# Optimization experiments

Hardware: AMD Instinct MI355X
Metric: run time of the kernel (lower is better)

The kernel has to match this reference:

```python
import jax, jax.numpy as jnp
import numpy as np

B, DIM, L, H, W = 4, 128, 256, 8, 8
N = L * H * W
D_INNER, D_STATE, D_CONV, DT_RANK = 128, 8, 4, 8


def _ln(x, w, b, eps=1e-5):
    m = x.mean(-1, keepdims=True)
    v = ((x - m) ** 2).mean(-1, keepdims=True)
    return (x - m) * jax.lax.rsqrt(v + eps) * w + b


def _mamba_fusion(x, z_in, p, i):
    # x, z_in: (B, N, DIM). x drives the SSM; z_in provides the cross-modal gate.
    u = x @ p['Wx'][i]                                    # (B, N, D_INNER)
    z = z_in @ p['Wz'][i]                                 # (B, N, D_INNER)
    # causal depthwise conv1d along tokens, kernel D_CONV (torch pad=k-1 then truncate)
    up = jnp.pad(u, ((0, 0), (D_CONV - 1, 0), (0, 0)))
    w = p['conv_w'][i]                                    # (D_INNER, D_CONV)
    uc = sum(up[:, k:k + u.shape[1], :] * w[:, k] for k in range(D_CONV)) + p['conv_b'][i]
    uc = jax.nn.silu(uc)
    x_dbl = uc @ p['Wxproj'][i]                           # (B, N, DT_RANK + 2*D_STATE)
    dt_r, Bm, Cm = jnp.split(x_dbl, [DT_RANK, DT_RANK + D_STATE], axis=-1)
    dt = jax.nn.softplus(dt_r @ p['Wdt'][i] + p['bdt'][i])  # (B, N, D_INNER)
    A = -jnp.exp(p['A_log'][i])                           # (D_INNER, D_STATE)
    dA = jnp.exp(dt[..., None] * A)                       # (B, N, D_INNER, D_STATE)
    dBu = dt[..., None] * Bm[:, :, None, :] * uc[..., None]

    def step(h, inp):
        dA_t, dBu_t, C_t = inp
        h = dA_t * h + dBu_t                              # (B, D_INNER, D_STATE)
        return h, jnp.einsum('bds,bs->bd', h, C_t)

    h0 = jnp.zeros((u.shape[0], D_INNER, D_STATE), u.dtype)
    _, ys = jax.lax.scan(step, h0, (dA.swapaxes(0, 1), dBu.swapaxes(0, 1), Cm.swapaxes(0, 1)))
    y = ys.swapaxes(0, 1) + p['Dp'][i] * uc
    y = y * jax.nn.silu(z)
    return y @ p['Wout_m'][i] + p['bout_m'][i]


def _cross_block(in0, in1, p, i):
    skip = in0
    a = _ln(in0, p['ln0_w'][i], p['ln0_b'][i])
    b = _ln(in1, p['ln1_w'][i], p['ln1_b'][i])
    return skip + _mamba_fusion(a, b, p, i)


def setup_inputs() -> dict:
    key = jax.random.key(0)
    ks = jax.random.split(key, 16)
    s_in = 1.0 / np.sqrt(DIM)
    s_di = 1.0 / np.sqrt(D_INNER)
    inp = {
        'front': jax.random.normal(ks[0], (B, DIM, L, H, W), jnp.float32),
        'back': jax.random.normal(ks[1], (B, DIM, L, H, W), jnp.float32),
        'ln0_w': jnp.ones((2, DIM), jnp.float32),
        'ln0_b': jnp.zeros((2, DIM), jnp.float32),
        'ln1_w': jnp.ones((2, DIM), jnp.float32),
        'ln1_b': jnp.zeros((2, DIM), jnp.float32),
        'Wx': jax.random.normal(ks[2], (2, DIM, D_INNER), jnp.float32) * s_in,
        'Wz': jax.random.normal(ks[3], (2, DIM, D_INNER), jnp.float32) * s_in,
        'conv_w': jax.random.normal(ks[4], (2, D_INNER, D_CONV), jnp.float32) * 0.5,
        'conv_b': jnp.zeros((2, D_INNER), jnp.float32),
        'Wxproj': jax.random.normal(ks[5], (2, D_INNER, DT_RANK + 2 * D_STATE), jnp.float32) * s_di,
        'Wdt': jax.random.normal(ks[6], (2, DT_RANK, D_INNER), jnp.float32) * (1.0 / np.sqrt(DT_RANK)),
        'bdt': jnp.full((2, D_INNER), -4.6, jnp.float32),  # softplus^-1(~0.01)
        'A_log': jnp.broadcast_to(jnp.log(jnp.arange(1, D_STATE + 1, dtype=jnp.float32)), (2, D_INNER, D_STATE)).copy(),
        'Dp': jnp.ones((2, D_INNER), jnp.float32),
        'Wout_m': jax.random.normal(ks[7], (2, D_INNER, DIM), jnp.float32) * s_di,
        'bout_m': jnp.zeros((2, DIM), jnp.float32),
        'Wout': jax.random.normal(ks[8], (DIM, DIM), jnp.float32) * s_in,
        'bout': jnp.zeros((DIM,), jnp.float32),
    }
    return inp


def reference(front, back, ln0_w, ln0_b, ln1_w, ln1_b, Wx, Wz, conv_w, conv_b,
              Wxproj, Wdt, bdt, A_log, Dp, Wout_m, bout_m, Wout, bout):
    p = dict(ln0_w=ln0_w, ln0_b=ln0_b, ln1_w=ln1_w, ln1_b=ln1_b, Wx=Wx, Wz=Wz,
             conv_w=conv_w, conv_b=conv_b, Wxproj=Wxproj, Wdt=Wdt, bdt=bdt,
             A_log=A_log, Dp=Dp, Wout_m=Wout_m, bout_m=bout_m)
    ff = front.reshape(B, DIM, N).swapaxes(1, 2)          # (B, N, DIM)
    bf = back.reshape(B, DIM, N).swapaxes(1, 2)
    f_fus = _cross_block(ff, bf, p, 0)
    b_fus = _cross_block(bf, ff, p, 1)
    fusion = ((f_fus + b_fus) * 0.5) @ Wout + bout
    return fusion.swapaxes(1, 2).reshape(B, DIM, L, H, W)
```

## Files before the change

### kernel.cpp

```cpp
#include <hip/hip_runtime.h>

#define DEV static __device__ __forceinline__

typedef short s16x8 __attribute__((ext_vector_type(8)));
typedef float f32x4 __attribute__((ext_vector_type(4)));
typedef unsigned short u16;

DEV float b2f(u16 u){ return __uint_as_float(((unsigned int)u) << 16); }
DEV u16 f2b(float f){
  unsigned int x = __float_as_uint(f);
  x += 0x7fffu + ((x >> 16) & 1u);
  return (u16)(x >> 16);
}
DEV float silu_f(float x){ return x * __builtin_amdgcn_rcpf(1.f + __expf(-x)); }
DEV float softplus_f(float x){ return (x > 15.f) ? x : __logf(1.f + __expf(x)); }
DEV bool detf32(const void* lnw){ return *(const unsigned int*)lnw == 0x3F800000u; }
DEV float ldin(const void* p, long long i, bool f){
  return f ? ((const float*)p)[i] : b2f(((const u16*)p)[i]);
}

static constexpr int BATCH = 4;
static constexpr int NSEQ  = 16384;
static constexpr int RTOT  = BATCH * NSEQ;
static constexpr int GCH   = 256;
static constexpr int DIRSZ = BATCH*GCH*128*8;

__global__ __launch_bounds__(256) void k_setup(
                        const void* ln0w, const void* ln0b, const void* ln1w, const void* ln1b,
                        const void* Wx, const void* Wz, const void* Wxp, const void* Wdt,
                        const void* bdt, const void* Alog, const void* convw, const void* convb,
                        const void* Dpr, const void* Woutm, const void* boutm,
                        const void* Wout, const void* bout,
                        u16* Wuz, u16* WdtBC, u16* Wcat, u16* WoutT,
                        float* buz, float* bdtf, float* bcat, float* boutf,
                        float* Aexp, float* convwF, float* convbF, float* DpF)
{
  bool f = detf32(ln0w);
  int tid = blockIdx.x * 256 + threadIdx.x;
  int gs  = gridDim.x * 256;
  for (int idx = tid; idx < 2*256*128; idx += gs){
    int d = idx >> 15; int n = (idx >> 7) & 255; int k = idx & 127;
    float wv;
    if (n < 128) wv = ldin(ln0w, d*128+k, f) * ldin(Wx, (long long)(d*128+k)*128 + n, f);
    else         wv = ldin(ln1w, (1-d)*128+k, f) * ldin(Wz, (long long)((1-d)*128+k)*128 + (n-128), f);
    Wuz[idx] = f2b(wv);
  }
  for (int idx = tid; idx < 2*256; idx += gs){
    int d = idx >> 8; int n = idx & 255;
    float s = 0.f;
    if (n < 128){
      for (int k = 0; k < 128; ++k)
        s += ldin(ln0b, d*128+k, f) * ldin(Wx, (long long)(d*128+k)*128 + n, f);
    } else {
      for (int k = 0; k < 128; ++k)
        s += ldin(ln1b, (1-d)*128+k, f) * ldin(Wz, (long long)((1-d)*128+k)*128 + (n-128), f);
    }
    buz[idx] = s;
  }
  for (int idx = tid; idx < 2*128; idx += gs)
    bdtf[idx] = ldin(bdt, idx, f);
  for (int idx = tid; idx < 2*144*128; idx += gs){
    int i = idx / (144*128); int rem = idx % (144*128); int n = rem >> 7; int k = rem & 127;
    if (n < 128){
      float s = 0.f;
      for (int j = 0; j < 8; ++j)
        s += ldin(Wxp, (long long)(i*128+k)*24 + j, f) * ldin(Wdt, (long long)(i*8+j)*128 + n, f);
      WdtBC[idx] = f2b(s);
    } else {
      WdtBC[idx] = f2b(ldin(Wxp, (long long)(i*128+k)*24 + (n - 120), f));
    }
  }
  for (int idx = tid; idx < 128*256; idx += gs){
    int n = idx >> 8; int k = idx & 255;
    Wcat[idx] = f2b(ldin(Woutm, (long long)k*128 + n, f));
  }
  for (int idx = tid; idx < 128*128; idx += gs){
    int n = idx >> 7, k = idx & 127;
    WoutT[idx] = f2b(ldin(Wout, (long long)k*128 + n, f));
  }
  for (int idx = tid; idx < 128; idx += gs){
    bcat[idx]  = ldin(boutm, idx, f) + ldin(boutm, 128 + idx, f);
    boutf[idx] = ldin(bout, idx, f);
  }
  for (int idx = tid; idx < 2*128*8; idx += gs)
    Aexp[idx] = -expf(ldin(Alog, idx, f));
  for (int idx = tid; idx < 2*128*4; idx += gs)
    convwF[idx] = ldin(convw, idx, f);
  for (int idx = tid; idx < 2*128; idx += gs){
    convbF[idx] = ldin(convb, idx, f);
    DpF[idx]   = ldin(Dpr, idx, f);
  }
}

__global__ __launch_bounds__(256) void k_ln(const void* front, const void* back, const void* ln0w,
                                            u16* xf, u16* xb, u16* sfbh)
{
  bool fF = detf32(ln0w);
  __shared__ u16 Af[64][130];
  __shared__ u16 Ab[64][130];
  __shared__ float Mf[64], Rf[64], Mb[64], Rb[64];
  int tid = threadIdx.x;
  long long r0 = (long long)blockIdx.x * 64;
  int b  = (int)(r0 >> 14);
  int n0 = (int)(r0 & 16383);
  if (fF){
    const float* fp = (const float*)front;
    const float* bp = (const float*)back;
    for (int it = 0; it < 8; ++it){
      int d = it*16 + (tid >> 4);
      int t = (tid & 15) * 4;
      long long gi = ((long long)(b*128 + d))*NSEQ + n0 + t;
      float4 vf = *(const float4*)&fp[gi];
      float4 vb = *(const float4*)&bp[gi];
      Af[t+0][d] = f2b(vf.x); Af[t+1][d] = f2b(vf.y);
      Af[t+2][d] = f2b(vf.z); Af[t+3][d] = f2b(vf.w);
      Ab[t+0][d] = f2b(vb.x); Ab[t+1][d] = f2b(vb.y);
      Ab[t+2][d] = f2b(vb.z); Ab[t+3][d] = f2b(vb.w);
    }
  } else {
    const u16* fp = (const u16*)front;
    const u16* bp = (const u16*)back;
    for (int it = 0; it < 4; ++it){
      int d = it*32 + (tid >> 3);
      int t = (tid & 7) * 8;
      long long gi = ((long long)(b*128 + d))*NSEQ + n0 + t;
      uint4 vf = *(const uint4*)&fp[gi];
      uint4 vb = *(const uint4*)&bp[gi];
      Af[t+0][d] = (u16)vf.x; Af[t+1][d] = (u16)(vf.x>>16);
      Af[t+2][d] = (u16)vf.y; Af[t+3][d] = (u16)(vf.y>>16);
      Af[t+4][d] = (u16)vf.z; Af[t+5][d] = (u16)(vf.z>>16);
      Af[t+6][d] = (u16)vf.w; Af[t+7][d] = (u16)(vf.w>>16);
      Ab[t+0][d] = (u16)vb.x; Ab[t+1][d] = (u16)(vb.x>>16);
      Ab[t+2][d] = (u16)vb.y; Ab[t+3][d] = (u16)(vb.y>>16);
      Ab[t+4][d] = (u16)vb.z; Ab[t+5][d] = (u16)(vb.z>>16);
      Ab[t+6][d] = (u16)vb.w; Ab[t+7][d] = (u16)(vb.w>>16);
    }
  }
  __syncthreads();
  {
    int t = tid >> 2, sub = tid & 3;
    float s = 0.f, ss = 0.f, s2 = 0.f, ss2 = 0.f;
    for (int k = 0; k < 32; ++k){
      float v = b2f(Af[t][sub*32 + k]); s  += v; ss  += v*v;
      float w = b2f(Ab[t][sub*32 + k]); s2 += w; ss2 += w*w;
    }
    for (int m = 1; m < 4; m <<= 1){
      s  += __shfl_xor(s,  m, 64); ss  += __shfl_xor(ss,  m, 64);
      s2 += __shfl_xor(s2, m, 64); ss2 += __shfl_xor(ss2, m, 64);
    }
    if (sub == 0){
      float mf = s  * (1.f/128.f); float vf = ss  * (1.f/128.f) - mf*mf;
      Mf[t] = mf; Rf[t] = rsqrtf(vf + 1e-5f);
      float mb = s2 * (1.f/128.f); float vb = ss2 * (1.f/128.f) - mb*mb;
      Mb[t] = mb; Rb[t] = rsqrtf(vb + 1e-5f);
    }
  }
  __syncthreads();
  for (int it = 0; it < 8; ++it){
    int t = it*8 + (tid >> 5);
    int c = (tid & 31) * 4;
    float mf = Mf[t], rf = Rf[t], mb = Mb[t], rb = Rb[t];
    float f0 = b2f(Af[t][c+0]), f1 = b2f(Af[t][c+1]), f2 = b2f(Af[t][c+2]), f3 = b2f(Af[t][c+3]);
    float g0 = b2f(Ab[t][c+0]), g1 = b2f(Ab[t][c+1]), g2 = b2f(Ab[t][c+2]), g3 = b2f(Ab[t][c+3]);
    ushort4 xo, zo, so;
    xo.x = f2b((f0-mf)*rf); xo.y = f2b((f1-mf)*rf); xo.z = f2b((f2-mf)*rf); xo.w = f2b((f3-mf)*rf);
    zo.x = f2b((g0-mb)*rb); zo.y = f2b((g1-mb)*rb); zo.z = f2b((g2-mb)*rb); zo.w = f2b((g3-mb)*rb);
    so.x = f2b(f0+g0); so.y = f2b(f1+g1); so.z = f2b(f2+g2); so.w = f2b(f3+g3);
    long long o = (r0 + t)*128 + c;
    *(ushort4*)&xf[o] = xo;
    *(ushort4*)&xb[o] = zo;
    *(ushort4*)&sfbh[o] = so;
  }
}

__global__ __launch_bounds__(256) void k_guz(const u16* __restrict__ xf,
                                             const u16* __restrict__ xb,
                                             const u16* __restrict__ Wuz,
                                             const float* __restrict__ buz,
                                             u16* __restrict__ u0, u16* __restrict__ u1,
                                             u16* __restrict__ z0, u16* __restrict__ z1)
{
  int dir = blockIdx.y;
  const u16* A = dir ? xb : xf;
  const u16* Wt = Wuz + dir*256*128;
  const float* bias = buz + dir*256;
  u16* outU = dir ? u1 : u0;
  u16* outZ = dir ? z0 : z1;
  __shared__ u16 Wl[256][72];
  __shared__ u16 Al[64][72];
  int tid = threadIdx.x;
  long long r0 = (long long)blockIdx.x * 64;
  int w = tid >> 6, lane = tid & 63;
  int q = lane >> 4, m = lane & 15;
  f32x4 acc[16];
  #pragma unroll
  for (int ct = 0; ct < 16; ++ct) acc[ct] = (f32x4){0.f,0.f,0.f,0.f};
  for (int kp = 0; kp < 2; ++kp){
    if (kp) __syncthreads();
    for (int ci = tid; ci < 256*8; ci += 256){
      int n = ci >> 3, c8 = ci & 7;
      *(uint4*)&Wl[n][c8*8] = *(const uint4*)&Wt[n*128 + kp*64 + c8*8];
    }
    for (int ci = tid; ci < 64*8; ci += 256){
      int rl = ci >> 3, c8 = ci & 7;
      *(uint4*)&Al[rl][c8*8] = *(const uint4*)&A[(r0 + rl)*128 + kp*64 + c8*8];
    }
    __syncthreads();
    #pragma unroll
    for (int kt = 0; kt < 2; ++kt){
      s16x8 af = *(const s16x8*)&Al[w*16 + m][kt*32 + q*8];
      #pragma unroll
      for (int ct = 0; ct < 16; ++ct){
        s16x8 bf = *(const s16x8*)&Wl[ct*16 + m][kt*32 + q*8];
        acc[ct] = __builtin_amdgcn_mfma_f32_16x16x32_bf16(af, bf, acc[ct], 0, 0, 0);
      }
    }
  }
  #pragma unroll
  for (int ct = 0; ct < 16; ++ct){
    int col = ct*16 + m;
    #pragma unroll
    for (int i = 0; i < 4; ++i){
      long long r = r0 + w*16 + q*4 + i;
      float v = acc[ct][i] + bias[col];
      if (col < 128) outU[r*128 + col] = f2b(v);
      else           outZ[r*128 + (col - 128)] = f2b(silu_f(v));
    }
  }
}

__global__ __launch_bounds__(256) void k_cps(const u16* __restrict__ u0p,
                                             const u16* __restrict__ u1p,
                                             const float* __restrict__ convwF,
                                             const float* __restrict__ convbF,
                                             const u16* __restrict__ WdtBC,
                                             const float* __restrict__ bdtf,
                                             const float* __restrict__ Aexp,
                                             u16* __restrict__ uc0p, u16* __restrict__ uc1p,
                                             u16* __restrict__ yg,
                                             float* __restrict__ BCg,
                                             float* __restrict__ P, float* __restrict__ Q)
{
  __shared__ u16 Al[64][136];
  __shared__ u16 Wl[144][136];
  __shared__ float BCl[64][16];
  int dir = blockIdx.y;
  const u16* u = dir ? u1p : u0p;
  u16* ucb = dir ? uc1p : uc0p;
  const u16* Wt = WdtBC + dir*18432;
  const float* bias = bdtf + dir*128;
  u16* dtb = yg + dir*128;
  float* BC = BCg + (long long)dir*RTOT*16;
  int tid = threadIdx.x;
  long long r0 = (long long)blockIdx.x * 64;
  int b  = (int)(r0 >> 14);
  int n0 = (int)(r0 & 16383);
  for (int ci = tid; ci < 144*16; ci += 256){
    int n = ci >> 4, c8 = ci & 15;
    *(uint4*)&Wl[n][c8*8] = *(const uint4*)&Wt[n*128 + c8*8];
  }
  {
    int c = tid & 127, h = tid >> 7;
    const float* wp = &convwF[(dir*128 + c)*4];
    float w0 = wp[0], w1 = wp[1], w2 = wp[2], w3 = wp[3];
    float cb = convbF[dir*128 + c];
    int t0 = h*32;
    const u16* up = u + (long long)b*NSEQ*128 + c;
    int nbase = n0 + t0;
    float win0 = (nbase-3 >= 0) ? b2f(up[(long long)(nbase-3)*128]) : 0.f;
    float win1 = (nbase-2 >= 0) ? b2f(up[(long long)(nbase-2)*128]) : 0.f;
    float win2 = (nbase-1 >= 0) ? b2f(up[(long long)(nbase-1)*128]) : 0.f;
    #pragma unroll
    for (int t = 0; t < 32; ++t){
      float cur = b2f(up[(long long)(nbase + t)*128]);
      float a = win0*w0 + win1*w1 + win2*w2 + cur*w3 + cb;
      u16 s = f2b(silu_f(a));
      Al[t0 + t][c] = s;
      ucb[(r0 + t0 + t)*128 + c] = s;
      win0 = win1; win1 = win2; win2 = cur;
    }
  }
  __syncthreads();
  int w = tid >> 6, lane = tid & 63;
  int q = lane >> 4, m = lane & 15;
  f32x4 acc[9];
  #pragma unroll
  for (int ct = 0; ct < 9; ++ct) acc[ct] = (f32x4){0.f,0.f,0.f,0.f};
  #pragma unroll
  for (int kt = 0; kt < 4; ++kt){
    s16x8 af = *(const s16x8*)&Al[w*16 + m][kt*32 + q*8];
    #pragma unroll
    for (int ct = 0; ct < 9; ++ct){
      s16x8 bf = *(const s16x8*)&Wl[ct*16 + m][kt*32 + q*8];
      acc[ct] = __builtin_amdgcn_mfma_f32_16x16x32_bf16(af, bf, acc[ct], 0, 0, 0);
    }
  }
  __syncthreads();
  u16* Dl = (u16*)&Wl[0][0];
  #pragma unroll
  for (int ct = 0; ct < 9; ++ct){
    int col = ct*16 + m;
    #pragma unroll
    for (int i = 0; i < 4; ++i){
      int rl = w*16 + q*4 + i;
      long long r = r0 + rl;
      float v = acc[ct][i];
      if (col < 128){
        u16 dv = f2b(softplus_f(v + bias[col]));
        dtb[r*256 + col] = dv;
        Dl[rl*136 + col] = dv;
      } else {
        BC[r*16 + (col - 128)] = v;
        BCl[rl][col - 128] = v;
      }
    }
  }
  __syncthreads();
  {
    int c = tid & 127, sh = tid >> 7;
    int g = (int)(r0 & 16383) >> 6;
    float Ac[4], Pr[4], H[4];
    #pragma unroll
    for (int j = 0; j < 4; ++j){
      Ac[j] = Aexp[(dir*128 + c)*8 + sh*4 + j];
      Pr[j] = 1.f; H[j] = 0.f;
    }
    for (int t = 0; t < 64; ++t){
      float d  = b2f(Dl[t*136 + c]);
      float uu = b2f(Al[t][c]);
      float du = d * uu;
      #pragma unroll
      for (int j = 0; j < 4; ++j){
        float dA = __expf(d * Ac[j]);
        H[j]  = dA*H[j] + du*BCl[t][sh*4 + j];
        Pr[j] *= dA;
      }
    }
    long long o = (long long)dir*DIRSZ + (((long long)b*GCH + g)*128 + c)*8 + sh*4;
    *(float4*)&P[o] = make_float4(Pr[0],Pr[1],Pr[2],Pr[3]);
    *(float4*)&Q[o] = make_float4(H[0],H[1],H[2],H[3]);
  }
}

__global__ __launch_bounds__(64) void k_scan2(const float* __restrict__ P,
                                              const float* __restrict__ Q,
                                              float* __restrict__ hinit)
{
  int idx = blockIdx.x*64 + threadIdx.x;
  int dir = idx >> 12;
  int rem = idx & 4095;
  int b  = rem >> 10;
  int cs = rem & 1023;
  long long base = (long long)dir*DIRSZ + (long long)b*GCH*1024 + cs;
  float h = 0.f;
  for (int g = 0; g < GCH; g += 8){
    long long o = base + (long long)g*1024;
    float p[8], qv[8];
    #pragma unroll
    for (int j = 0; j < 8; ++j){ p[j] = P[o + j*1024]; qv[j] = Q[o + j*1024]; }
    #pragma unroll
    for (int j = 0; j < 8; ++j){
      hinit[o + j*1024] = h;
      h = p[j]*h + qv[j];
    }
  }
}

__global__ __launch_bounds__(256) void k_scan3(const u16* __restrict__ uc0p,
                                               const u16* __restrict__ uc1p,
                                               const float* __restrict__ BCg,
                                               const float* __restrict__ hinit,
                                               const u16* __restrict__ z0p,
                                               const u16* __restrict__ z1p,
                                               const float* __restrict__ DpF,
                                               const float* __restrict__ Aexp,
                                               u16* yg)
{
  __shared__ float Bl[128][8];
  __shared__ float Cl[128][8];
  int dir = blockIdx.y;
  const u16* uc = dir ? uc1p : uc0p;
  const u16* zs = dir ? z1p : z0p;
  const float* BC = BCg + (long long)dir*RTOT*16;
  int tid = threadIdx.x;
  int gp = blockIdx.x & 127;
  int b  = blockIdx.x >> 7;
  long long tokbase = (long long)b*NSEQ + gp*128;
  for (int idx = tid; idx < 128*8; idx += 256){
    int row = idx >> 3, s = idx & 7;
    Bl[row][s] = BC[(tokbase + row)*16 + s];
    Cl[row][s] = BC[(tokbase + row)*16 + 8 + s];
  }
  __syncthreads();
  int c = tid & 127;
  int gh = tid >> 7;
  int g = gp*2 + gh;
  int doff = dir*128;
  float Ac[8], H[8];
  long long ho = (long long)dir*DIRSZ + (((long long)b*GCH + g)*128 + c)*8;
  float4 h0 = *(const float4*)&hinit[ho];
  float4 h1 = *(const float4*)&hinit[ho + 4];
  H[0]=h0.x; H[1]=h0.y; H[2]=h0.z; H[3]=h0.w;
  H[4]=h1.x; H[5]=h1.y; H[6]=h1.z; H[7]=h1.w;
  #pragma unroll
  for (int s = 0; s < 8; ++s) Ac[s] = Aexp[(dir*128 + c)*8 + s];
  float dpc = DpF[dir*128 + c];
  long long rbase = (long long)b*NSEQ + g*64;
  for (int t = 0; t < 64; ++t){
    long long r = rbase + t;
    float d  = b2f(yg[r*256 + doff + c]);
    float uu = b2f(uc[r*128 + c]);
    float du = d * uu;
    int rowl = gh*64 + t;
    float y = 0.f;
    #pragma unroll
    for (int s = 0; s < 8; ++s){
      float dA = __expf(d * Ac[s]);
      H[s] = dA*H[s] + du*Bl[rowl][s];
      y += H[s]*Cl[rowl][s];
    }
    float zv = b2f(zs[r*128 + c]);
    yg[r*256 + doff + c] = f2b((y + dpc*uu) * zv);
  }
}

__global__ __launch_bounds__(256) void k_tail(const u16* __restrict__ yg,
                                              const u16* __restrict__ Wcat,
                                              const float* __restrict__ bcat,
                                              const u16* __restrict__ sfbh,
                                              const u16* __restrict__ WoutT,
                                              const float* __restrict__ boutf,
                                              void* outp, const void* dflag)
{
  __shared__ u16 Wl[128][136];
  __shared__ u16 Al[64][136];
  __shared__ u16 Sl[64][136];
  int tid = threadIdx.x;
  long long r0 = (long long)blockIdx.x * 64;
  int w = tid >> 6, lane = tid & 63;
  int q = lane >> 4, m = lane & 15;
  f32x4 acc[8];
  #pragma unroll
  for (int ct = 0; ct < 8; ++ct) acc[ct] = (f32x4){0.f,0.f,0.f,0.f};
  for (int kp = 0; kp < 2; ++kp){
    if (kp) __syncthreads();
    for (int ci = tid; ci < 128*16; ci += 256){
      int n = ci >> 4, c8 = ci & 15;
      *(uint4*)&Wl[n][c8*8] = *(const uint4*)&Wcat[n*256 + kp*128 + c8*8];
    }
    for (int ci = tid; ci < 64*16; ci += 256){
      int rl = ci >> 4, c8 = ci & 15;
      *(uint4*)&Al[rl][c8*8] = *(const uint4*)&yg[(r0 + rl)*256 + kp*128 + c8*8];
    }
    __syncthreads();
    #pragma unroll
    for (int kt = 0; kt < 4; ++kt){
      s16x8 af = *(const s16x8*)&Al[w*16 + m][kt*32 + q*8];
      #pragma unroll
      for (int ct = 0; ct < 8; ++ct){
        s16x8 bf = *(const s16x8*)&Wl[ct*16 + m][kt*32 + q*8];
        acc[ct] = __builtin_amdgcn_mfma_f32_16x16x32_bf16(af, bf, acc[ct], 0, 0, 0);
      }
    }
  }
  #pragma unroll
  for (int ct = 0; ct < 8; ++ct){
    int col = ct*16 + m;
    #pragma unroll
    for (int i = 0; i < 4; ++i){
      int rl = w*16 + q*4 + i;
      long long r = r0 + rl;
      Sl[rl][col] = f2b(acc[ct][i] + bcat[col] + b2f(sfbh[r*128 + col]));
    }
  }
  __syncthreads();
  for (int ci = tid; ci < 128*16; ci += 256){
    int n = ci >> 4, c8 = ci & 15;
    *(uint4*)&Wl[n][c8*8] = *(const uint4*)&WoutT[n*128 + c8*8];
  }
  __syncthreads();
  f32x4 acc2[8];
  #pragma unroll
  for (int ct = 0; ct < 8; ++ct) acc2[ct] = (f32x4){0.f,0.f,0.f,0.f};
  #pragma unroll
  for (int kt = 0; kt < 4; ++kt){
    s16x8 af = *(const s16x8*)&Sl[w*16 + m][kt*32 + q*8];
    #pragma unroll
    for (int ct = 0; ct < 8; ++ct){
      s16x8 bf = *(const s16x8*)&Wl[ct*16 + m][kt*32 + q*8];
      acc2[ct] = __builtin_amdgcn_mfma_f32_16x16x32_bf16(af, bf, acc2[ct], 0, 0, 0);
    }
  }
  u16* Tl = &Al[0][0];
  #pragma unroll
  for (int ct = 0; ct < 8; ++ct){
    int col = ct*16 + m;
    #pragma unroll
    for (int i = 0; i < 4; ++i){
      int rl = w*16 + q*4 + i;
      Tl[col*68 + rl] = f2b(0.5f*acc2[ct][i] + boutf[col]);
    }
  }
  __syncthreads();
  long long b = r0 >> 14; long long tok0 = r0 & 16383;
  bool fo = detf32(dflag);
  if (fo){
    float* of = (float*)outp;
    for (int idx = tid; idx < 128*16; idx += 256){
      int n = idx >> 4; int t0 = (idx & 15)*4;
      float4 v;
      v.x = b2f(Tl[n*68 + t0+0]); v.y = b2f(Tl[n*68 + t0+1]);
      v.z = b2f(Tl[n*68 + t0+2]); v.w = b2f(Tl[n*68 + t0+3]);
      *(float4*)&of[(((long long)(b*128 + n)) << 14) + tok0 + t0] = v;
    }
  } else {
    u16* ob = (u16*)outp;
    for (int idx = tid; idx < 128*16; idx += 256){
      int n = idx >> 4; int t0 = (idx & 15)*4;
      ushort4 v;
      v.x = Tl[n*68 + t0+0]; v.y = Tl[n*68 + t0+1];
      v.z = Tl[n*68 + t0+2]; v.w = Tl[n*68 + t0+3];
      *(ushort4*)&ob[(((long long)(b*128 + n)) << 14) + tok0 + t0] = v;
    }
  }
}

extern "C" void kernel_launch(void* const* d_in, const int* in_sizes, int n_in,
                              void* d_out, int out_size, void* d_ws, size_t ws_size,
                              hipStream_t stream)
{
  (void)in_sizes; (void)n_in; (void)out_size; (void)ws_size;
  const void* front = d_in[0];
  const void* back  = d_in[1];
  const void* ln0w  = d_in[2];
  const void* ln0b  = d_in[3];
  const void* ln1w  = d_in[4];
  const void* ln1b  = d_in[5];
  const void* Wx    = d_in[6];
  const void* Wz    = d_in[7];
  const void* convw = d_in[8];
  const void* convb = d_in[9];
  const void* Wxp   = d_in[10];
  const void* Wdt   = d_in[11];
  const void* bdt   = d_in[12];
  const void* Alog  = d_in[13];
  const void* Dpr   = d_in[14];
  const void* Woutm = d_in[15];
  const void* boutm = d_in[16];
  const void* Wout  = d_in[17];
  const void* bout  = d_in[18];

  char* p = (char*)d_ws;
  auto alloc = [&](size_t bytes) -> void* {
    void* q = (void*)p; p += (bytes + 255) & ~(size_t)255; return q;
  };
  u16*   xf    = (u16*)  alloc((size_t)RTOT*128*2);
  u16*   xb    = (u16*)  alloc((size_t)RTOT*128*2);
  u16*   sfbh  = (u16*)  alloc((size_t)RTOT*128*2);
  u16*   u0    = (u16*)  alloc((size_t)RTOT*128*2);
  u16*   u1    = (u16*)  alloc((size_t)RTOT*128*2);
  u16*   z0    = (u16*)  alloc((size_t)RTOT*128*2);
  u16*   z1    = (u16*)  alloc((size_t)RTOT*128*2);
  float* BC    = (float*)alloc((size_t)2*RTOT*16*4);
  float* Pb    = (float*)alloc((size_t)2*DIRSZ*4);
  float* Qb    = (float*)alloc((size_t)2*DIRSZ*4);
  float* hin   = (float*)alloc((size_t)2*DIRSZ*4);
  u16*   yg    = (u16*)  alloc((size_t)RTOT*256*2);
  u16*   Wuz   = (u16*)  alloc(2*256*128*2);
  u16*   WdtBC = (u16*)  alloc(2*144*128*2);
  u16*   Wcat  = (u16*)  alloc(128*256*2);
  u16*   WoutT = (u16*)  alloc(128*128*2);
  float* buz   = (float*)alloc(2*256*4);
  float* bdtf  = (float*)alloc(2*128*4);
  float* bcat  = (float*)alloc(128*4);
  float* boutf = (float*)alloc(128*4);
  float* Aexp  = (float*)alloc(2*128*8*4);
  float* convwF= (float*)alloc(2*128*4*4);
  float* convbF= (float*)alloc(2*128*4);
  float* DpF   = (float*)alloc(2*128*4);

  k_setup<<<128,256,0,stream>>>(ln0w,ln0b,ln1w,ln1b,Wx,Wz,Wxp,Wdt,bdt,Alog,convw,convb,Dpr,
                                Woutm,boutm,Wout,bout,
                                Wuz,WdtBC,Wcat,WoutT,buz,bdtf,bcat,boutf,Aexp,
                                convwF,convbF,DpF);
  k_ln<<<RTOT/64,256,0,stream>>>(front,back,ln0w,xf,xb,sfbh);

  dim3 g2(RTOT/64, 2);
  k_guz<<<g2,256,0,stream>>>(xf, xb, Wuz, buz, u0, u1, z0, z1);
  k_cps<<<g2,256,0,stream>>>(u0, u1, convwF, convbF, WdtBC, bdtf, Aexp,
                             xf, xb, yg, BC, Pb, Qb);
  k_scan2<<<128,64,0,stream>>>(Pb, Qb, hin);
  dim3 g3(BATCH*GCH/2, 2);
  k_scan3<<<g3,256,0,stream>>>(xf, xb, BC, hin, z0, z1, DpF, Aexp, yg);
  k_tail<<<RTOT/64,256,0,stream>>>(yg, Wcat, bcat, sfbh, WoutT, boutf, d_out, ln0w);
}
```

Baseline: 346.7 us.

## Replace per-state exps with powers of one exp when A matches S4D init

Both scan kernels check at runtime whether A equals -(s+1) for every state. If it does, they compute exp(-dt) once and build every decay factor from its powers, replacing eight exponentials per step with one exp and a few multiplies. Otherwise they fall back to the original path. k_cps also stops staging the weight matrix in shared memory and loads MFMA operands directly from global, which shrinks LDS use, and it adds an occupancy hint. The risks are small rounding differences from the power products and possibly slower weight loads from global memory.

```diff
diff --git a/kernel.cpp b/kernel.cpp
--- a/kernel.cpp
+++ b/kernel.cpp
@@ -229,7 +229,7 @@
   }
 }
 
-__global__ __launch_bounds__(256) void k_cps(const u16* __restrict__ u0p,
+__global__ __launch_bounds__(256, 4) void k_cps(const u16* __restrict__ u0p,
                                              const u16* __restrict__ u1p,
                                              const float* __restrict__ convwF,
                                              const float* __restrict__ convbF,
@@ -242,7 +242,7 @@
                                              float* __restrict__ P, float* __restrict__ Q)
 {
   __shared__ u16 Al[64][136];
-  __shared__ u16 Wl[144][136];
+  __shared__ u16 Dl[64][136];
   __shared__ float BCl[64][16];
   int dir = blockIdx.y;
   const u16* u = dir ? u1p : u0p;
@@ -255,10 +255,6 @@
   long long r0 = (long long)blockIdx.x * 64;
   int b  = (int)(r0 >> 14);
   int n0 = (int)(r0 & 16383);
-  for (int ci = tid; ci < 144*16; ci += 256){
-    int n = ci >> 4, c8 = ci & 15;
-    *(uint4*)&Wl[n][c8*8] = *(const uint4*)&Wt[n*128 + c8*8];
-  }
   {
     int c = tid & 127, h = tid >> 7;
     const float* wp = &convwF[(dir*128 + c)*4];
@@ -289,14 +285,13 @@
   #pragma unroll
   for (int kt = 0; kt < 4; ++kt){
     s16x8 af = *(const s16x8*)&Al[w*16 + m][kt*32 + q*8];
+    const u16* wrow = Wt + m*128 + kt*32 + q*8;
     #pragma unroll
     for (int ct = 0; ct < 9; ++ct){
-      s16x8 bf = *(const s16x8*)&Wl[ct*16 + m][kt*32 + q*8];
+      s16x8 bf = *(const s16x8*)&wrow[ct*16*128];
       acc[ct] = __builtin_amdgcn_mfma_f32_16x16x32_bf16(af, bf, acc[ct], 0, 0, 0);
     }
   }
-  __syncthreads();
-  u16* Dl = (u16*)&Wl[0][0];
   #pragma unroll
   for (int ct = 0; ct < 9; ++ct){
     int col = ct*16 + m;
@@ -308,7 +303,7 @@
       if (col < 128){
         u16 dv = f2b(softplus_f(v + bias[col]));
         dtb[r*256 + col] = dv;
-        Dl[rl*136 + col] = dv;
+        Dl[rl][col] = dv;
       } else {
         BC[r*16 + (col - 128)] = v;
         BCl[rl][col - 128] = v;
@@ -319,24 +314,43 @@
   {
     int c = tid & 127, sh = tid >> 7;
     int g = (int)(r0 & 16383) >> 6;
+    int base = sh*4;
     float Ac[4], Pr[4], H[4];
+    bool fast = true;
     #pragma unroll
     for (int j = 0; j < 4; ++j){
-      Ac[j] = Aexp[(dir*128 + c)*8 + sh*4 + j];
+      Ac[j] = Aexp[(dir*128 + c)*8 + base + j];
+      fast = fast && (fabsf(Ac[j] + (float)(base + j + 1)) < 2e-4f);
       Pr[j] = 1.f; H[j] = 0.f;
     }
-    for (int t = 0; t < 64; ++t){
-      float d  = b2f(Dl[t*136 + c]);
-      float uu = b2f(Al[t][c]);
-      float du = d * uu;
-      #pragma unroll
-      for (int j = 0; j < 4; ++j){
-        float dA = __expf(d * Ac[j]);
-        H[j]  = dA*H[j] + du*BCl[t][sh*4 + j];
-        Pr[j] *= dA;
+    if (fast){
+      for (int t = 0; t < 64; ++t){
+        float d  = b2f(Dl[t][c]);
+        float uu = b2f(Al[t][c]);
+        float du = d * uu;
+        float E  = __expf(-d);
+        float E2 = E*E, E3 = E2*E, E4 = E2*E2;
+        float M  = base ? E4 : 1.f;
+        float dA0 = M*E, dA1 = M*E2, dA2 = M*E3, dA3 = M*E4;
+        H[0] = dA0*H[0] + du*BCl[t][base+0]; Pr[0] *= dA0;
+        H[1] = dA1*H[1] + du*BCl[t][base+1]; Pr[1] *= dA1;
+        H[2] = dA2*H[2] + du*BCl[t][base+2]; Pr[2] *= dA2;
+        H[3] = dA3*H[3] + du*BCl[t][base+3]; Pr[3] *= dA3;
       }
-    }
-    long long o = (long long)dir*DIRSZ + (((long long)b*GCH + g)*128 + c)*8 + sh*4;
+    } else {
+      for (int t = 0; t < 64; ++t){
+        float d  = b2f(Dl[t][c]);
+        float uu = b2f(Al[t][c]);
+        float du = d * uu;
+        #pragma unroll
+        for (int j = 0; j < 4; ++j){
+          float dA = __expf(d * Ac[j]);
+          H[j]  = dA*H[j] + du*BCl[t][base + j];
+          Pr[j] *= dA;
+        }
+      }
+    }
+    long long o = (long long)dir*DIRSZ + (((long long)b*GCH + g)*128 + c)*8 + base;
     *(float4*)&P[o] = make_float4(Pr[0],Pr[1],Pr[2],Pr[3]);
     *(float4*)&Q[o] = make_float4(H[0],H[1],H[2],H[3]);
   }
@@ -402,25 +416,50 @@
   float4 h1 = *(const float4*)&hinit[ho + 4];
   H[0]=h0.x; H[1]=h0.y; H[2]=h0.z; H[3]=h0.w;
   H[4]=h1.x; H[5]=h1.y; H[6]=h1.z; H[7]=h1.w;
-  #pragma unroll
-  for (int s = 0; s < 8; ++s) Ac[s] = Aexp[(dir*128 + c)*8 + s];
+  bool fast = true;
+  #pragma unroll
+  for (int s = 0; s < 8; ++s){
+    Ac[s] = Aexp[(dir*128 + c)*8 + s];
+    fast = fast && (fabsf(Ac[s] + (float)(s + 1)) < 2e-4f);
+  }
   float dpc = DpF[dir*128 + c];
   long long rbase = (long long)b*NSEQ + g*64;
-  for (int t = 0; t < 64; ++t){
-    long long r = rbase + t;
-    float d  = b2f(yg[r*256 + doff + c]);
-    float uu = b2f(uc[r*128 + c]);
-    float du = d * uu;
-    int rowl = gh*64 + t;
-    float y = 0.f;
-    #pragma unroll
-    for (int s = 0; s < 8; ++s){
-      float dA = __expf(d * Ac[s]);
-      H[s] = dA*H[s] + du*Bl[rowl][s];
-      y += H[s]*Cl[rowl][s];
-    }
-    float zv = b2f(zs[r*128 + c]);
-    yg[r*256 + doff + c] = f2b((y + dpc*uu) * zv);
+  if (fast){
+    for (int t = 0; t < 64; ++t){
+      long long r = rbase + t;
+      float d  = b2f(yg[r*256 + doff + c]);
+      float uu = b2f(uc[r*128 + c]);
+      float du = d * uu;
+      int rowl = gh*64 + t;
+      float E  = __expf(-d);
+      float E2 = E*E, E3 = E2*E, E4 = E2*E2;
+      float dA[8] = {E, E2, E3, E4, E4*E, E4*E2, E4*E3, E4*E4};
+      float y = 0.f;
+      #pragma unroll
+      for (int s = 0; s < 8; ++s){
+        H[s] = dA[s]*H[s] + du*Bl[rowl][s];
+        y += H[s]*Cl[rowl][s];
+      }
+      float zv = b2f(zs[r*128 + c]);
+      yg[r*256 + doff + c] = f2b((y + dpc*uu) * zv);
+    }
+  } else {
+    for (int t = 0; t < 64; ++t){
+      long long r = rbase + t;
+      float d  = b2f(yg[r*256 + doff + c]);
+      float uu = b2f(uc[r*128 + c]);
+      float du = d * uu;
+      int rowl = gh*64 + t;
+      float y = 0.f;
+      #pragma unroll
+      for (int s = 0; s < 8; ++s){
+        float dA = __expf(d * Ac[s]);
+        H[s] = dA*H[s] + du*Bl[rowl][s];
+        y += H[s]*Cl[rowl][s];
+      }
+      float zv = b2f(zs[r*128 + c]);
+      yg[r*256 + doff + c] = f2b((y + dpc*uu) * zv);
+    }
   }
 }
 
```

After: 339.7 us. 2.0% less time.
